# Kernel tuning notes

Hardware: AMD Instinct MI355X
Metric: run time of the kernel (lower is better)

## Reference

```python
import jax, jax.numpy as jnp
import numpy as np

NEG_BIG = -9e15
ALPHA = 0.2  # leakyrelu negative slope


def setup_inputs() -> dict:
    key = jax.random.key(0)
    k1, k2, k3, k4 = jax.random.split(key, 4)
    N, F_in, F_out = 8192, 256, 256
    h = jax.random.normal(k1, (N, F_in), dtype=jnp.float32)
    adj = jax.random.randint(k2, (N, N), 0, 2).astype(jnp.float32)
    W = jax.random.normal(k3, (F_in, F_out), dtype=jnp.float32) * (1.414 / np.sqrt(F_in))
    a = jax.random.normal(k4, (2 * F_out, 1), dtype=jnp.float32) * (1.414 / np.sqrt(2 * F_out))
    return {"h": h, "adj": adj, "W": W, "a": a}


def reference(h, adj, W, a):
    F_out = W.shape[1]
    Wh = h @ W  # [N, F_out]
    # Decomposed additive score: e_ij = leakyrelu(a1.Wh_i + a2.Wh_j)
    # identical to matmul(cat([Wh_i, Wh_j]), a) in the original.
    a1 = a[:F_out, 0]  # [F_out]
    a2 = a[F_out:, 0]  # [F_out]
    s1 = Wh @ a1  # [N]
    s2 = Wh @ a2  # [N]
    e = jax.nn.leaky_relu(s1[:, None] + s2[None, :], negative_slope=ALPHA)  # [N, N]
    e = jnp.where(adj > 0, e, NEG_BIG)
    attention = jax.nn.softmax(e, axis=1)
    # dropout skipped (eval mode: training=False)
    h_prime = attention @ Wh  # [N, F_out]
    return jax.nn.elu(h_prime)
```

## Files before the change

kernel.cpp:

```cpp
#include <hip/hip_runtime.h>
#include <hip/hip_bf16.h>

#define N 8192
#define F 256
#define KSPLIT 8
#define JBLK (N / KSPLIT)
#define NITER (JBLK / 32)
#define LOG2E 1.4426950408889634f

using s16x8 = __attribute__((ext_vector_type(8))) short;
using f32x4 = __attribute__((ext_vector_type(4))) float;

static __device__ __forceinline__ unsigned short f2bf(float f) {
  unsigned int u = __float_as_uint(f);
  unsigned int r = u + 0x7fffu + ((u >> 16) & 1u);
  return (unsigned short)(r >> 16);
}
static __device__ __forceinline__ float bf2f(unsigned short u) {
  return __uint_as_float(((unsigned int)u) << 16);
}
static __device__ __forceinline__ void glds16(const void* g, void* l) {
  __builtin_amdgcn_global_load_lds(
      (const __attribute__((address_space(1))) unsigned int*)g,
      (__attribute__((address_space(3))) unsigned int*)l, 16, 0, 0);
}

__global__ __launch_bounds__(256) void k0_wt(const float* __restrict__ W,
                                             unsigned short* __restrict__ Wt) {
  int k = blockIdx.x;
  int f = threadIdx.x;
  Wt[f * 256 + k] = f2bf(W[k * 256 + f]);
}

__global__ __launch_bounds__(256) void k1_wh(const float* __restrict__ h,
                                             const unsigned short* __restrict__ Wt,
                                             const float* __restrict__ a,
                                             char* __restrict__ WhbT,
                                             float* __restrict__ s1g,
                                             float* __restrict__ s2g) {
  __shared__ char lds[8192 + 32768];
  char* Alds = lds;
  char* Blds = lds + 8192;
  int t = threadIdx.x;
  int i0 = blockIdx.x * 64;
  int l = t & 63, w = t >> 6;
  int lr = l & 15, lk = l >> 4;
  f32x4 acc[4][4] = {};
  for (int kt = 0; kt < 4; ++kt) {
    int k0 = kt * 64;
    if (kt) __syncthreads();
#pragma unroll
    for (int c = 0; c < 4; ++c) {
      int flat = c * 256 + t;
      int i = flat >> 4, jc = flat & 15;
      float4 v = *reinterpret_cast<const float4*>(h + (size_t)(i0 + i) * 256 + k0 + jc * 4);
      ushort4 pk;
      pk.x = f2bf(v.x); pk.y = f2bf(v.y); pk.z = f2bf(v.z); pk.w = f2bf(v.w);
      *reinterpret_cast<ushort4*>(Alds + i * 128 + ((jc * 8) ^ ((i & 7) << 4))) = pk;
    }
#pragma unroll
    for (int c = 0; c < 8; ++c) {
      int idx = c * 256 + t;
      int fr = idx >> 3, kc = idx & 7;
      uint4 v = *reinterpret_cast<const uint4*>(Wt + fr * 256 + k0 + kc * 8);
      *reinterpret_cast<uint4*>(Blds + fr * 128 + ((kc * 16) ^ ((fr & 7) << 4))) = v;
    }
    __syncthreads();
#pragma unroll
    for (int kk = 0; kk < 2; ++kk) {
      int kofs = kk * 64 + lk * 16;
      s16x8 afr[4], bfr[4];
#pragma unroll
      for (int mf = 0; mf < 4; ++mf) {
        int ar = mf * 16 + lr;
        afr[mf] = *reinterpret_cast<const s16x8*>(Alds + ar * 128 + (kofs ^ ((ar & 7) << 4)));
      }
#pragma unroll
      for (int nf = 0; nf < 4; ++nf) {
        int br = w * 64 + nf * 16 + lr;
        bfr[nf] = *reinterpret_cast<const s16x8*>(Blds + br * 128 + (kofs ^ ((br & 7) << 4)));
      }
#pragma unroll
      for (int mf = 0; mf < 4; ++mf)
#pragma unroll
        for (int nf = 0; nf < 4; ++nf)
          acc[mf][nf] = __builtin_amdgcn_mfma_f32_16x16x32_bf16(afr[mf], bfr[nf], acc[mf][nf], 0, 0, 0);
    }
  }
#pragma unroll
  for (int mf = 0; mf < 4; ++mf) {
#pragma unroll
    for (int nf = 0; nf < 4; ++nf) {
      int f = w * 64 + nf * 16 + lr;
      int tj32 = blockIdx.x * 2 + (mf >> 1);
      int g = ((mf & 1) << 1) + (lk >> 1);
      int sub = lk & 1;
      int fp = f >> 1;
      int u = ((((f & 1) << 2) + g) ^ (fp & 7));
      ushort4 pk;
      pk.x = f2bf(acc[mf][nf][0]);
      pk.y = f2bf(acc[mf][nf][1]);
      pk.z = f2bf(acc[mf][nf][2]);
      pk.w = f2bf(acc[mf][nf][3]);
      *reinterpret_cast<ushort4*>(WhbT + (size_t)tj32 * 16384 + fp * 128 + u * 16 + sub * 8) = pk;
    }
  }
  float a1v[4], a2v[4];
#pragma unroll
  for (int nf = 0; nf < 4; ++nf) {
    int f = w * 64 + nf * 16 + lr;
    a1v[nf] = a[f];
    a2v[nf] = a[256 + f];
  }
  float* s1l = (float*)lds;
  float* s2l = s1l + 64;
  __syncthreads();
  if (t < 128) s1l[t] = 0.f;
  __syncthreads();
#pragma unroll
  for (int mf = 0; mf < 4; ++mf) {
#pragma unroll
    for (int r = 0; r < 4; ++r) {
      float p1 = 0.f, p2 = 0.f;
#pragma unroll
      for (int nf = 0; nf < 4; ++nf) {
        p1 += acc[mf][nf][r] * a1v[nf];
        p2 += acc[mf][nf][r] * a2v[nf];
      }
      p1 += __shfl_xor(p1, 1); p1 += __shfl_xor(p1, 2);
      p1 += __shfl_xor(p1, 4); p1 += __shfl_xor(p1, 8);
      p2 += __shfl_xor(p2, 1); p2 += __shfl_xor(p2, 2);
      p2 += __shfl_xor(p2, 4); p2 += __shfl_xor(p2, 8);
      if (lr == 0) {
        atomicAdd(&s1l[mf * 16 + lk * 4 + r], p1);
        atomicAdd(&s2l[mf * 16 + lk * 4 + r], p2);
      }
    }
  }
  __syncthreads();
  if (t < 64) {
    s1g[i0 + t] = s1l[t] * LOG2E;
    s2g[i0 + t] = s2l[t] * LOG2E;
  }
}

__global__ __launch_bounds__(512) void k3_attn(const float* __restrict__ adj,
                                               const char* __restrict__ WhbT,
                                               const float* __restrict__ s1,
                                               const float* __restrict__ s2,
                                               float* __restrict__ numw,
                                               float* __restrict__ denw) {
  __shared__ char lds[2 * 16384 + 2 * 16384 + 4096];
  char* Abase = lds;
  char* Bbase = lds + 32768;
  float* s2l = (float*)(lds + 65536);
  int t = threadIdx.x, w = t >> 6, l = t & 63, lr = l & 15, lk = l >> 4;
  int i0 = blockIdx.x * 128;
  int ks = blockIdx.y;
  int jb = ks * JBLK;
  int row = i0 + w * 16 + lr;
  float s1v = s1[row];

  *reinterpret_cast<float2*>(&s2l[t * 2]) = *reinterpret_cast<const float2*>(s2 + jb + t * 2);

  f32x4 acc[16] = {};
  float ds = 0.f;

#define STAGE(tile, buf)                                                        \
  {                                                                             \
    const char* gB = WhbT + (size_t)(ks * NITER + (tile)) * 16384 + w * 2048;   \
    char* lB = Bbase + (buf) * 16384 + w * 2048;                                \
    _Pragma("unroll") for (int c = 0; c < 2; ++c)                               \
        glds16(gB + c * 1024 + l * 16, lB + c * 1024);                          \
    char* lA = Abase + (buf) * 16384 + w * 2048;                                \
    _Pragma("unroll") for (int c = 0; c < 2; ++c) {                             \
      int lr8 = c * 8 + (l >> 3);                                               \
      const float* srcA = adj + (size_t)(i0 + w * 16 + lr8) * N + jb +          \
                          (tile) * 32 + (((l & 7) ^ (lr8 & 7)) << 2);           \
      glds16(srcA, lA + c * 1024);                                              \
    }                                                                           \
  }

  STAGE(0, 0);
  __syncthreads();

  for (int it = 0; it < NITER; ++it) {
    int cb = it & 1;
    if (it + 1 < NITER) {
      STAGE(it + 1, cb ^ 1);
      asm volatile("s_waitcnt vmcnt(4)" ::: "memory");
    } else {
      asm volatile("s_waitcnt vmcnt(0)" ::: "memory");
    }
    __builtin_amdgcn_s_barrier();

    const char* At = Abase + cb * 16384 + w * 2048 + lr * 128;
    f32x4 av0 = *reinterpret_cast<const f32x4*>(At + (((lk << 1) ^ (lr & 7)) << 4));
    f32x4 av1 = *reinterpret_cast<const f32x4*>(At + ((((lk << 1) | 1) ^ (lr & 7)) << 4));
    const float* sp = &s2l[it * 32 + lk * 8];
    float4 sv0 = *reinterpret_cast<const float4*>(sp);
    float4 sv1 = *reinterpret_cast<const float4*>(sp + 4);
    s16x8 afr;
#define PEL(e, av, sv)                                                          \
    {                                                                           \
      float x = s1v + (sv); x = fmaxf(x, 0.2f * x);                             \
      float p = (av) > 0.f ? exp2f(x) : 0.f;                                    \
      unsigned short us = (unsigned short)((__float_as_uint(p) + 0x8000u) >> 16); \
      ds += bf2f(us); afr[e] = (short)us;                                       \
    }
    PEL(0, av0[0], sv0.x) PEL(1, av0[1], sv0.y) PEL(2, av0[2], sv0.z) PEL(3, av0[3], sv0.w)
    PEL(4, av1[0], sv1.x) PEL(5, av1[1], sv1.y) PEL(6, av1[2], sv1.z) PEL(7, av1[3], sv1.w)
#undef PEL

    const char* Bt = Bbase + cb * 16384;
#pragma unroll
    for (int nf = 0; nf < 16; ++nf) {
      int br = nf * 16 + lr;
      int fp = br >> 1;
      int u = ((((br & 1) << 2) + lk) ^ (fp & 7));
      s16x8 bfr = *reinterpret_cast<const s16x8*>(Bt + fp * 128 + u * 16);
      acc[nf] = __builtin_amdgcn_mfma_f32_16x16x32_bf16(afr, bfr, acc[nf], 0, 0, 0);
    }
    asm volatile("s_waitcnt lgkmcnt(0)" ::: "memory");
    __builtin_amdgcn_s_barrier();
  }
#undef STAGE

  ds += __shfl_xor(ds, 16);
  ds += __shfl_xor(ds, 32);
  if (l < 16) denw[(size_t)ks * N + row] = ds;

  float* nump = numw + (size_t)ks * N * F;
#pragma unroll
  for (int nf = 0; nf < 16; ++nf) {
#pragma unroll
    for (int rr = 0; rr < 4; ++rr) {
      nump[(size_t)(i0 + w * 16 + lk * 4 + rr) * F + nf * 16 + lr] = acc[nf][rr];
    }
  }
}

__global__ __launch_bounds__(256) void k4_fin(const float* __restrict__ numw,
                                              const float* __restrict__ denw,
                                              float* __restrict__ out) {
  int idx = (blockIdx.x * 256 + threadIdx.x) * 4;
  int i = idx >> 8;
  float4 sn = {0.f, 0.f, 0.f, 0.f};
  float sd = 0.f;
#pragma unroll
  for (int ksp = 0; ksp < KSPLIT; ++ksp) {
    float4 v = *reinterpret_cast<const float4*>(numw + (size_t)ksp * N * F + idx);
    sn.x += v.x; sn.y += v.y; sn.z += v.z; sn.w += v.w;
    sd += denw[(size_t)ksp * N + i];
  }
  float r = 1.f / sd;
  float4 o;
  float hp;
  hp = sn.x * r; o.x = hp > 0.f ? hp : (__expf(hp) - 1.f);
  hp = sn.y * r; o.y = hp > 0.f ? hp : (__expf(hp) - 1.f);
  hp = sn.z * r; o.z = hp > 0.f ? hp : (__expf(hp) - 1.f);
  hp = sn.w * r; o.w = hp > 0.f ? hp : (__expf(hp) - 1.f);
  *reinterpret_cast<float4*>(out + idx) = o;
}

extern "C" void kernel_launch(void* const* d_in, const int* in_sizes, int n_in,
                              void* d_out, int out_size, void* d_ws, size_t ws_size,
                              hipStream_t stream) {
  const float* h   = (const float*)d_in[0];
  const float* adj = (const float*)d_in[1];
  const float* W   = (const float*)d_in[2];
  const float* a   = (const float*)d_in[3];
  float* out = (float*)d_out;

  char* ws = (char*)d_ws;
  size_t o = 0;
  char* WhbT           = ws + o;                    o += (size_t)4 * 1024 * 1024;
  float* s1            = (float*)(ws + o);          o += 32768;
  float* s2            = (float*)(ws + o);          o += 32768;
  float* denw          = (float*)(ws + o);          o += (size_t)KSPLIT * N * 4;
  unsigned short* Wt   = (unsigned short*)(ws + o); o += 131072;
  float* numw          = (float*)(ws + o);          o += (size_t)KSPLIT * N * F * 4;

  hipLaunchKernelGGL(k0_wt, dim3(256), dim3(256), 0, stream, W, Wt);
  hipLaunchKernelGGL(k1_wh, dim3(N / 64), dim3(256), 0, stream, h, Wt, a, WhbT, s1, s2);
  hipLaunchKernelGGL(k3_attn, dim3(N / 128, KSPLIT), dim3(512), 0, stream,
                     adj, WhbT, s1, s2, numw, denw);
  hipLaunchKernelGGL(k4_fin, dim3(N * F / 1024), dim3(256), 0, stream, numw, denw, out);
}
```

Measured before the change: 133.9 us.

## Double rows per block in attention kernel and deepen to triple-buffered pipeline

Each wave now processes 32 rows (two 16-row MFMA tiles) instead of 16, so every Wh B-fragment loaded from LDS feeds two MFMAs and B tile global traffic is halved. The global->LDS staging goes from double to triple buffering, with two tiles prefetched ahead and matching vmcnt waits. The trade-off is doubled accumulator registers (32 f32x4 per lane), about 150KB of LDS per block, and half as many blocks (256 instead of 512), which may hurt occupancy and latency hiding.

```diff
diff --git a/kernel.cpp b/kernel.cpp
--- a/kernel.cpp
+++ b/kernel.cpp
@@ -150,92 +150,111 @@
                                                const float* __restrict__ s2,
                                                float* __restrict__ numw,
                                                float* __restrict__ denw) {
-  __shared__ char lds[2 * 16384 + 2 * 16384 + 4096];
+  __shared__ char lds[3 * 32768 + 3 * 16384 + 4096];
   char* Abase = lds;
-  char* Bbase = lds + 32768;
-  float* s2l = (float*)(lds + 65536);
+  char* Bbase = lds + 98304;
+  float* s2l = (float*)(lds + 147456);
   int t = threadIdx.x, w = t >> 6, l = t & 63, lr = l & 15, lk = l >> 4;
-  int i0 = blockIdx.x * 128;
+  int i0 = blockIdx.x * 256;
   int ks = blockIdx.y;
   int jb = ks * JBLK;
-  int row = i0 + w * 16 + lr;
-  float s1v = s1[row];
+  int rowA = i0 + w * 32 + lr;
+  int rowB = rowA + 16;
+  float s1vA = s1[rowA], s1vB = s1[rowB];
 
   *reinterpret_cast<float2*>(&s2l[t * 2]) = *reinterpret_cast<const float2*>(s2 + jb + t * 2);
 
-  f32x4 acc[16] = {};
-  float ds = 0.f;
+  f32x4 acc0[16] = {}, acc1[16] = {};
+  float dsA = 0.f, dsB = 0.f;
 
 #define STAGE(tile, buf)                                                        \
   {                                                                             \
     const char* gB = WhbT + (size_t)(ks * NITER + (tile)) * 16384 + w * 2048;   \
     char* lB = Bbase + (buf) * 16384 + w * 2048;                                \
-    _Pragma("unroll") for (int c = 0; c < 2; ++c)                               \
-        glds16(gB + c * 1024 + l * 16, lB + c * 1024);                          \
-    char* lA = Abase + (buf) * 16384 + w * 2048;                                \
-    _Pragma("unroll") for (int c = 0; c < 2; ++c) {                             \
-      int lr8 = c * 8 + (l >> 3);                                               \
-      const float* srcA = adj + (size_t)(i0 + w * 16 + lr8) * N + jb +          \
-                          (tile) * 32 + (((l & 7) ^ (lr8 & 7)) << 2);           \
+    glds16(gB + l * 16, lB);                                                    \
+    glds16(gB + 1024 + l * 16, lB + 1024);                                      \
+    char* lA = Abase + (buf) * 32768 + w * 4096;                                \
+    _Pragma("unroll") for (int c = 0; c < 4; ++c) {                             \
+      int rloc = w * 32 + c * 8 + (l >> 3);                                     \
+      const float* srcA = adj + (size_t)(i0 + rloc) * N + jb +                  \
+                          (tile) * 32 + (((l & 7) ^ (rloc & 7)) << 2);          \
       glds16(srcA, lA + c * 1024);                                              \
     }                                                                           \
   }
 
   STAGE(0, 0);
+  STAGE(1, 1);
   __syncthreads();
 
   for (int it = 0; it < NITER; ++it) {
-    int cb = it & 1;
-    if (it + 1 < NITER) {
-      STAGE(it + 1, cb ^ 1);
-      asm volatile("s_waitcnt vmcnt(4)" ::: "memory");
+    int buf = it % 3;
+    if (it + 2 < NITER) {
+      STAGE(it + 2, (buf + 2) % 3);
+      asm volatile("s_waitcnt vmcnt(12)" ::: "memory");
+    } else if (it + 1 < NITER) {
+      asm volatile("s_waitcnt vmcnt(6)" ::: "memory");
     } else {
       asm volatile("s_waitcnt vmcnt(0)" ::: "memory");
     }
     __builtin_amdgcn_s_barrier();
 
-    const char* At = Abase + cb * 16384 + w * 2048 + lr * 128;
-    f32x4 av0 = *reinterpret_cast<const f32x4*>(At + (((lk << 1) ^ (lr & 7)) << 4));
-    f32x4 av1 = *reinterpret_cast<const f32x4*>(At + ((((lk << 1) | 1) ^ (lr & 7)) << 4));
+    const char* At = Abase + buf * 32768 + w * 4096;
+    int sw0 = ((2 * lk) ^ (lr & 7)) << 4;
+    int sw1 = ((2 * lk + 1) ^ (lr & 7)) << 4;
+    f32x4 avA0 = *reinterpret_cast<const f32x4*>(At + lr * 128 + sw0);
+    f32x4 avA1 = *reinterpret_cast<const f32x4*>(At + lr * 128 + sw1);
+    f32x4 avB0 = *reinterpret_cast<const f32x4*>(At + (lr + 16) * 128 + sw0);
+    f32x4 avB1 = *reinterpret_cast<const f32x4*>(At + (lr + 16) * 128 + sw1);
     const float* sp = &s2l[it * 32 + lk * 8];
     float4 sv0 = *reinterpret_cast<const float4*>(sp);
     float4 sv1 = *reinterpret_cast<const float4*>(sp + 4);
-    s16x8 afr;
-#define PEL(e, av, sv)                                                          \
+    s16x8 afA, afB;
+#define PEL(dst, e, av, sv, s1p, dsx)                                           \
     {                                                                           \
-      float x = s1v + (sv); x = fmaxf(x, 0.2f * x);                             \
+      float x = (s1p) + (sv); x = fmaxf(x, 0.2f * x);                           \
       float p = (av) > 0.f ? exp2f(x) : 0.f;                                    \
       unsigned short us = (unsigned short)((__float_as_uint(p) + 0x8000u) >> 16); \
-      ds += bf2f(us); afr[e] = (short)us;                                       \
-    }
-    PEL(0, av0[0], sv0.x) PEL(1, av0[1], sv0.y) PEL(2, av0[2], sv0.z) PEL(3, av0[3], sv0.w)
-    PEL(4, av1[0], sv1.x) PEL(5, av1[1], sv1.y) PEL(6, av1[2], sv1.z) PEL(7, av1[3], sv1.w)
+      dsx += bf2f(us); dst[e] = (short)us;                                      \
+    }
+    PEL(afA, 0, avA0[0], sv0.x, s1vA, dsA) PEL(afA, 1, avA0[1], sv0.y, s1vA, dsA)
+    PEL(afA, 2, avA0[2], sv0.z, s1vA, dsA) PEL(afA, 3, avA0[3], sv0.w, s1vA, dsA)
+    PEL(afA, 4, avA1[0], sv1.x, s1vA, dsA) PEL(afA, 5, avA1[1], sv1.y, s1vA, dsA)
+    PEL(afA, 6, avA1[2], sv1.z, s1vA, dsA) PEL(afA, 7, avA1[3], sv1.w, s1vA, dsA)
+    PEL(afB, 0, avB0[0], sv0.x, s1vB, dsB) PEL(afB, 1, avB0[1], sv0.y, s1vB, dsB)
+    PEL(afB, 2, avB0[2], sv0.z, s1vB, dsB) PEL(afB, 3, avB0[3], sv0.w, s1vB, dsB)
+    PEL(afB, 4, avB1[0], sv1.x, s1vB, dsB) PEL(afB, 5, avB1[1], sv1.y, s1vB, dsB)
+    PEL(afB, 6, avB1[2], sv1.z, s1vB, dsB) PEL(afB, 7, avB1[3], sv1.w, s1vB, dsB)
 #undef PEL
 
-    const char* Bt = Bbase + cb * 16384;
+    const char* Bt = Bbase + buf * 16384;
 #pragma unroll
     for (int nf = 0; nf < 16; ++nf) {
       int br = nf * 16 + lr;
       int fp = br >> 1;
       int u = ((((br & 1) << 2) + lk) ^ (fp & 7));
       s16x8 bfr = *reinterpret_cast<const s16x8*>(Bt + fp * 128 + u * 16);
-      acc[nf] = __builtin_amdgcn_mfma_f32_16x16x32_bf16(afr, bfr, acc[nf], 0, 0, 0);
+      acc0[nf] = __builtin_amdgcn_mfma_f32_16x16x32_bf16(afA, bfr, acc0[nf], 0, 0, 0);
+      acc1[nf] = __builtin_amdgcn_mfma_f32_16x16x32_bf16(afB, bfr, acc1[nf], 0, 0, 0);
     }
     asm volatile("s_waitcnt lgkmcnt(0)" ::: "memory");
     __builtin_amdgcn_s_barrier();
   }
 #undef STAGE
 
-  ds += __shfl_xor(ds, 16);
-  ds += __shfl_xor(ds, 32);
-  if (l < 16) denw[(size_t)ks * N + row] = ds;
-
+  dsA += __shfl_xor(dsA, 16); dsA += __shfl_xor(dsA, 32);
+  dsB += __shfl_xor(dsB, 16); dsB += __shfl_xor(dsB, 32);
+  if (l < 16) {
+    denw[(size_t)ks * N + rowA] = dsA;
+    denw[(size_t)ks * N + rowB] = dsB;
+  }
   float* nump = numw + (size_t)ks * N * F;
 #pragma unroll
   for (int nf = 0; nf < 16; ++nf) {
 #pragma unroll
     for (int rr = 0; rr < 4; ++rr) {
-      nump[(size_t)(i0 + w * 16 + lk * 4 + rr) * F + nf * 16 + lr] = acc[nf][rr];
+      int irow = i0 + w * 32 + lk * 4 + rr;
+      nump[(size_t)irow * F + nf * 16 + lr] = acc0[nf][rr];
+      nump[(size_t)(irow + 16) * F + nf * 16 + lr] = acc1[nf][rr];
     }
   }
 }
@@ -283,7 +302,7 @@
 
   hipLaunchKernelGGL(k0_wt, dim3(256), dim3(256), 0, stream, W, Wt);
   hipLaunchKernelGGL(k1_wh, dim3(N / 64), dim3(256), 0, stream, h, Wt, a, WhbT, s1, s2);
-  hipLaunchKernelGGL(k3_attn, dim3(N / 128, KSPLIT), dim3(512), 0, stream,
+  hipLaunchKernelGGL(k3_attn, dim3(N / 256, KSPLIT), dim3(512), 0, stream,
                      adj, WhbT, s1, s2, numw, denw);
   hipLaunchKernelGGL(k4_fin, dim3(N * F / 1024), dim3(256), 0, stream, numw, denw, out);
 }
```

Result: slower. 143.2 us (+7.0%).

## Precompute adjacency bitmask and stream bits instead of fp32 adj in attention

Applied to the files above, without the earlier changes.

Adds a pre-pass kernel that packs the fp32 adjacency matrix into a 1-bit-per-entry mask using wave shuffles. The attention kernel then reads one mask word per tile instead of staging 32 fp32 adj columns per row into LDS. This halves the attention kernel's LDS footprint and removes adj loads and LDS reads from its inner loop. In exchange, the full adj read moves into a separate serial pass that can no longer overlap with MFMA compute, and the mask adds extra write and read traffic.

```diff
diff --git a/kernel.cpp b/kernel.cpp
--- a/kernel.cpp
+++ b/kernel.cpp
@@ -23,6 +23,33 @@
   __builtin_amdgcn_global_load_lds(
       (const __attribute__((address_space(1))) unsigned int*)g,
       (__attribute__((address_space(3))) unsigned int*)l, 16, 0, 0);
+}
+
+__global__ __launch_bounds__(256) void k_mask(const float* __restrict__ adj,
+                                              unsigned int* __restrict__ mask) {
+  int tid = blockIdx.x * 256 + threadIdx.x;
+  int l = threadIdx.x & 63;
+  const int STRIDE = 2048 * 256;
+#pragma unroll
+  for (int p = 0; p < 8; ++p) {
+    float4 v[4];
+#pragma unroll
+    for (int j = 0; j < 4; ++j) {
+      size_t q = (size_t)(p * 4 + j) * STRIDE + tid;
+      v[j] = *reinterpret_cast<const float4*>(adj + q * 4);
+    }
+#pragma unroll
+    for (int j = 0; j < 4; ++j) {
+      size_t q = (size_t)(p * 4 + j) * STRIDE + tid;
+      float bs = v[j].x + 2.f * v[j].y + 4.f * v[j].z + 8.f * v[j].w;
+      unsigned int nib = (unsigned int)(int)bs;
+      unsigned int word = 0;
+#pragma unroll
+      for (int e = 0; e < 8; ++e)
+        word |= ((unsigned int)__shfl((int)nib, (l & 56) + e, 64)) << (4 * e);
+      if ((l & 7) == 0) mask[q >> 3] = word;
+    }
+  }
 }
 
 __global__ __launch_bounds__(256) void k0_wt(const float* __restrict__ W,
@@ -144,72 +171,66 @@
   }
 }
 
-__global__ __launch_bounds__(512) void k3_attn(const float* __restrict__ adj,
+__global__ __launch_bounds__(512) void k3_attn(const unsigned int* __restrict__ mask,
                                                const char* __restrict__ WhbT,
                                                const float* __restrict__ s1,
                                                const float* __restrict__ s2,
                                                float* __restrict__ numw,
                                                float* __restrict__ denw) {
-  __shared__ char lds[2 * 16384 + 2 * 16384 + 4096];
-  char* Abase = lds;
-  char* Bbase = lds + 32768;
-  float* s2l = (float*)(lds + 65536);
+  __shared__ char lds[2 * 16384 + 4096];
+  char* Bbase = lds;
+  float* s2l = (float*)(lds + 32768);
   int t = threadIdx.x, w = t >> 6, l = t & 63, lr = l & 15, lk = l >> 4;
   int i0 = blockIdx.x * 128;
   int ks = blockIdx.y;
   int jb = ks * JBLK;
   int row = i0 + w * 16 + lr;
   float s1v = s1[row];
+  const unsigned int* mrow = mask + (size_t)row * (N / 32) + (jb >> 5);
 
   *reinterpret_cast<float2*>(&s2l[t * 2]) = *reinterpret_cast<const float2*>(s2 + jb + t * 2);
 
   f32x4 acc[16] = {};
   float ds = 0.f;
 
-#define STAGE(tile, buf)                                                        \
+#define STAGE_B(tile, buf)                                                      \
   {                                                                             \
     const char* gB = WhbT + (size_t)(ks * NITER + (tile)) * 16384 + w * 2048;   \
     char* lB = Bbase + (buf) * 16384 + w * 2048;                                \
-    _Pragma("unroll") for (int c = 0; c < 2; ++c)                               \
-        glds16(gB + c * 1024 + l * 16, lB + c * 1024);                          \
-    char* lA = Abase + (buf) * 16384 + w * 2048;                                \
-    _Pragma("unroll") for (int c = 0; c < 2; ++c) {                             \
-      int lr8 = c * 8 + (l >> 3);                                               \
-      const float* srcA = adj + (size_t)(i0 + w * 16 + lr8) * N + jb +          \
-                          (tile) * 32 + (((l & 7) ^ (lr8 & 7)) << 2);           \
-      glds16(srcA, lA + c * 1024);                                              \
-    }                                                                           \
-  }
-
-  STAGE(0, 0);
+    glds16(gB + l * 16, lB);                                                    \
+    glds16(gB + 1024 + l * 16, lB + 1024);                                      \
+  }
+
+  unsigned int mwc = mrow[0];
+  STAGE_B(0, 0);
   __syncthreads();
 
   for (int it = 0; it < NITER; ++it) {
     int cb = it & 1;
+    unsigned int mwn = 0;
     if (it + 1 < NITER) {
-      STAGE(it + 1, cb ^ 1);
-      asm volatile("s_waitcnt vmcnt(4)" ::: "memory");
+      STAGE_B(it + 1, cb ^ 1);
+      mwn = mrow[it + 1];
+      asm volatile("s_waitcnt vmcnt(3)" ::: "memory");
     } else {
       asm volatile("s_waitcnt vmcnt(0)" ::: "memory");
     }
     __builtin_amdgcn_s_barrier();
 
-    const char* At = Abase + cb * 16384 + w * 2048 + lr * 128;
-    f32x4 av0 = *reinterpret_cast<const f32x4*>(At + (((lk << 1) ^ (lr & 7)) << 4));
-    f32x4 av1 = *reinterpret_cast<const f32x4*>(At + ((((lk << 1) | 1) ^ (lr & 7)) << 4));
     const float* sp = &s2l[it * 32 + lk * 8];
     float4 sv0 = *reinterpret_cast<const float4*>(sp);
     float4 sv1 = *reinterpret_cast<const float4*>(sp + 4);
+    unsigned int mb = mwc >> (lk * 8);
     s16x8 afr;
-#define PEL(e, av, sv)                                                          \
+#define PEL(e, sv)                                                              \
     {                                                                           \
       float x = s1v + (sv); x = fmaxf(x, 0.2f * x);                             \
-      float p = (av) > 0.f ? exp2f(x) : 0.f;                                    \
+      float p = ((mb >> (e)) & 1u) ? exp2f(x) : 0.f;                            \
       unsigned short us = (unsigned short)((__float_as_uint(p) + 0x8000u) >> 16); \
       ds += bf2f(us); afr[e] = (short)us;                                       \
     }
-    PEL(0, av0[0], sv0.x) PEL(1, av0[1], sv0.y) PEL(2, av0[2], sv0.z) PEL(3, av0[3], sv0.w)
-    PEL(4, av1[0], sv1.x) PEL(5, av1[1], sv1.y) PEL(6, av1[2], sv1.z) PEL(7, av1[3], sv1.w)
+    PEL(0, sv0.x) PEL(1, sv0.y) PEL(2, sv0.z) PEL(3, sv0.w)
+    PEL(4, sv1.x) PEL(5, sv1.y) PEL(6, sv1.z) PEL(7, sv1.w)
 #undef PEL
 
     const char* Bt = Bbase + cb * 16384;
@@ -223,8 +244,9 @@
     }
     asm volatile("s_waitcnt lgkmcnt(0)" ::: "memory");
     __builtin_amdgcn_s_barrier();
-  }
-#undef STAGE
+    mwc = mwn;
+  }
+#undef STAGE_B
 
   ds += __shfl_xor(ds, 16);
   ds += __shfl_xor(ds, 32);
@@ -279,11 +301,13 @@
   float* s2            = (float*)(ws + o);          o += 32768;
   float* denw          = (float*)(ws + o);          o += (size_t)KSPLIT * N * 4;
   unsigned short* Wt   = (unsigned short*)(ws + o); o += 131072;
+  unsigned int* mask   = (unsigned int*)(ws + o);   o += (size_t)N * (N / 32) * 4;
   float* numw          = (float*)(ws + o);          o += (size_t)KSPLIT * N * F * 4;
 
+  hipLaunchKernelGGL(k_mask, dim3(2048), dim3(256), 0, stream, adj, mask);
   hipLaunchKernelGGL(k0_wt, dim3(256), dim3(256), 0, stream, W, Wt);
   hipLaunchKernelGGL(k1_wh, dim3(N / 64), dim3(256), 0, stream, h, Wt, a, WhbT, s1, s2);
   hipLaunchKernelGGL(k3_attn, dim3(N / 128, KSPLIT), dim3(512), 0, stream,
-                     adj, WhbT, s1, s2, numw, denw);
+                     mask, WhbT, s1, s2, numw, denw);
   hipLaunchKernelGGL(k4_fin, dim3(N * F / 1024), dim3(256), 0, stream, numw, denw, out);
 }
```

Result: slower. 157.0 us (+17.3%).
